# Kernel tuning notes

Hardware: AMD Instinct MI355X
Metric: run time of the kernel (lower is better)

The kernel has to match this reference:

```python
import jax, jax.numpy as jnp
import numpy as np

N = 100000      # nodes
E = 1_600_000   # edges
IN = 128        # in_channels
OUT = 64        # out_channels


def _glorot(k, shape):
    lim = float(np.sqrt(6.0 / (shape[0] + shape[1])))
    return jax.random.uniform(k, shape, jnp.float32, -lim, lim)


def setup_inputs() -> dict:
    key = jax.random.key(0)
    ks = jax.random.split(key, 8)
    x = jax.random.normal(ks[0], (N, IN), jnp.float32)
    edge_index = jax.random.randint(ks[1], (2, E), 0, N, jnp.int32)
    eps = jax.random.normal(ks[2], (N, OUT), jnp.float32)
    return {
        "x": x,
        "edge_index": edge_index,
        "eps": eps,
        "W1": _glorot(ks[3], (IN, OUT)),
        "b1": jnp.zeros((OUT,), jnp.float32),
        "Wmu": _glorot(ks[4], (OUT, OUT)),
        "bmu": jnp.zeros((OUT,), jnp.float32),
        "Wlv": _glorot(ks[5], (OUT, OUT)),
        "blv": jnp.zeros((OUT,), jnp.float32),
        "Wdec": _glorot(ks[6], (OUT, IN)),
        "bdec": jnp.zeros((IN,), jnp.float32),
    }


def gcn_conv(x, W, b, src, dst, n):
    """PyG GCNConv: add self-loops, D^-1/2 (A+I) D^-1/2 X W + b."""
    h = x @ W  # [N, F] transform before aggregation (small F)
    deg = jax.ops.segment_sum(jnp.ones((src.shape[0],), h.dtype), dst,
                              num_segments=n) + 1.0  # +1 for self-loop
    dinv = jax.lax.rsqrt(deg)  # [N]
    norm = dinv[src] * dinv[dst]  # [E]
    msgs = h[src] * norm[:, None]  # [E, F] gather + scale
    agg = jax.ops.segment_sum(msgs, dst, num_segments=n)
    agg = agg + h * (dinv * dinv)[:, None]  # self-loop contribution
    return agg + b


def reference(x, edge_index, eps, W1, b1, Wmu, bmu, Wlv, blv, Wdec, bdec):
    src, dst = edge_index[0], edge_index[1]
    n = x.shape[0]
    h = jax.nn.relu(gcn_conv(x, W1, b1, src, dst, n))
    mu = gcn_conv(h, Wmu, bmu, src, dst, n)
    logvar = gcn_conv(h, Wlv, blv, src, dst, n)
    z = mu + eps * jnp.exp(logvar)  # training-mode reparameterize (std = exp(logvar), per source)
    recon = jax.nn.sigmoid(z @ Wdec + bdec)
    return recon, mu, logvar
```

## Files before the change

### kernel.cpp

```cpp
#include <hip/hip_runtime.h>


static __host__ __device__ inline size_t ws_align(size_t x) { return (x + 255) & ~size_t(255); }

__global__ void k_deg(const int* __restrict__ dst, int E, int* __restrict__ deg) {
    int e = blockIdx.x * blockDim.x + threadIdx.x;
    if (e < E) atomicAdd(&deg[dst[e]], 1);
}

__global__ void k_dinv(const int* __restrict__ deg, int N, float* __restrict__ dinv) {
    int i = blockIdx.x * blockDim.x + threadIdx.x;
    if (i < N) dinv[i] = rsqrtf((float)(deg[i] + 1));
}

__global__ void k_scan_partial(const int* __restrict__ deg, int N, int* __restrict__ part) {
    __shared__ int s[256];
    int t = threadIdx.x;
    int i = blockIdx.x * 256 + t;
    s[t] = (i < N) ? deg[i] : 0;
    __syncthreads();
    for (int off = 128; off > 0; off >>= 1) {
        if (t < off) s[t] += s[t + off];
        __syncthreads();
    }
    if (t == 0) part[blockIdx.x] = s[0];
}

__global__ void k_scan_top(const int* __restrict__ part, int nb, int* __restrict__ scanned) {
    __shared__ int s[512];
    int t = threadIdx.x;
    int v = (t < nb) ? part[t] : 0;
    s[t] = v;
    __syncthreads();
    for (int off = 1; off < 512; off <<= 1) {
        int x = 0;
        if (t >= off) x = s[t - off];
        __syncthreads();
        s[t] += x;
        __syncthreads();
    }
    if (t < nb) scanned[t] = s[t] - v;
}

__global__ void k_scan_down(const int* __restrict__ deg, int N, int E,
                            const int* __restrict__ scanned, int* __restrict__ offsets) {
    __shared__ int s[256];
    int t = threadIdx.x;
    int i = blockIdx.x * 256 + t;
    int v = (i < N) ? deg[i] : 0;
    s[t] = v;
    __syncthreads();
    for (int off = 1; off < 256; off <<= 1) {
        int x = 0;
        if (t >= off) x = s[t - off];
        __syncthreads();
        s[t] += x;
        __syncthreads();
    }
    if (i < N) offsets[i] = scanned[blockIdx.x] + s[t] - v;
    if (blockIdx.x == 0 && t == 0) offsets[N] = E;
}

__global__ void k_scatter(const int* __restrict__ src, const int* __restrict__ dst, int E,
                          int* __restrict__ cursor, int* __restrict__ src_sorted) {
    int e = blockIdx.x * blockDim.x + threadIdx.x;
    if (e < E) {
        int slot = atomicAdd(&cursor[dst[e]], 1);
        src_sorted[slot] = src[e];
    }
}

__global__ __launch_bounds__(256) void k_gemm_in(const float* __restrict__ X,
                                                 const float* __restrict__ W,
                                                 const float* __restrict__ dinv, int N,
                                                 float* __restrict__ C) {
    __shared__ float Ws[128 * 64];
    __shared__ float Xs[16][128];
    int t = threadIdx.x;
    const float4* W4 = (const float4*)W;
    float4* Ws4 = (float4*)Ws;
#pragma unroll
    for (int j = 0; j < 8; j++) Ws4[t + 256 * j] = W4[t + 256 * j];
    int row0 = blockIdx.x * 16;
    const float4* X4 = (const float4*)(X + (size_t)row0 * 128);
    float4* Xs4 = (float4*)&Xs[0][0];
#pragma unroll
    for (int j = 0; j < 2; j++) Xs4[t + 256 * j] = X4[t + 256 * j];
    __syncthreads();
    int r = t >> 4;
    int c0 = (t & 15) * 4;
    float a0 = 0.f, a1 = 0.f, a2 = 0.f, a3 = 0.f;
#pragma unroll 4
    for (int k = 0; k < 128; k++) {
        float xv = Xs[r][k];
        float4 w = *(const float4*)&Ws[k * 64 + c0];
        a0 += xv * w.x; a1 += xv * w.y; a2 += xv * w.z; a3 += xv * w.w;
    }
    float dv = dinv[row0 + r];
    float4 out = {a0 * dv, a1 * dv, a2 * dv, a3 * dv};
    *(float4*)(C + (size_t)(row0 + r) * 64 + c0) = out;
}

template <bool FIRST>
__global__ __launch_bounds__(256) void k_agg(const float* __restrict__ Hs,
                                             const float* __restrict__ dinv,
                                             const int* __restrict__ offsets,
                                             const int* __restrict__ src_sorted,
                                             const float* __restrict__ bias, int N,
                                             float* __restrict__ out) {
    int node = blockIdx.x * 4 + (threadIdx.x >> 6);
    int lane = threadIdx.x & 63;
    if (node >= N) return;
    float dv = dinv[node];
    int beg = offsets[node], end = offsets[node + 1];
    int nu = __builtin_amdgcn_readfirstlane(node);
    float acc = Hs[(size_t)nu * 64 + lane];
    float acc2 = 0.f;
    int j = beg;
    for (; j + 4 <= end; j += 4) {
        int s0 = __builtin_amdgcn_readfirstlane(src_sorted[j + 0]);
        int s1 = __builtin_amdgcn_readfirstlane(src_sorted[j + 1]);
        int s2 = __builtin_amdgcn_readfirstlane(src_sorted[j + 2]);
        int s3 = __builtin_amdgcn_readfirstlane(src_sorted[j + 3]);
        float h0 = Hs[(size_t)s0 * 64 + lane];
        float h1 = Hs[(size_t)s1 * 64 + lane];
        float h2 = Hs[(size_t)s2 * 64 + lane];
        float h3 = Hs[(size_t)s3 * 64 + lane];
        acc += h0 + h1;
        acc2 += h2 + h3;
    }
    for (; j < end; j++) {
        int s = __builtin_amdgcn_readfirstlane(src_sorted[j]);
        acc += Hs[(size_t)s * 64 + lane];
    }
    acc += acc2;
    float v;
    if (FIRST) {
        v = dv * acc + bias[lane];
        v = fmaxf(v, 0.f) * dv;
    } else {
        v = dv * acc;
    }
    out[(size_t)node * 64 + lane] = v;
}

__global__ __launch_bounds__(256) void k_muvz(const float* __restrict__ AGG,
                                              const float* __restrict__ Wmu,
                                              const float* __restrict__ bmu,
                                              const float* __restrict__ Wlv,
                                              const float* __restrict__ blv,
                                              const float* __restrict__ EPS, int N,
                                              float* __restrict__ mu_out,
                                              float* __restrict__ lv_out,
                                              float* __restrict__ z_out) {
    __shared__ float Wm[64 * 64];
    __shared__ float Wl[64 * 64];
    __shared__ float As[16][64];
    int t = threadIdx.x;
#pragma unroll
    for (int j = 0; j < 4; j++) {
        ((float4*)Wm)[t + 256 * j] = ((const float4*)Wmu)[t + 256 * j];
        ((float4*)Wl)[t + 256 * j] = ((const float4*)Wlv)[t + 256 * j];
    }
    int row0 = blockIdx.x * 16;
    ((float4*)&As[0][0])[t] = ((const float4*)(AGG + (size_t)row0 * 64))[t];
    __syncthreads();
    int r = t >> 4;
    int c0 = (t & 15) * 4;
    float m0 = 0.f, m1 = 0.f, m2 = 0.f, m3 = 0.f;
    float l0 = 0.f, l1 = 0.f, l2 = 0.f, l3 = 0.f;
#pragma unroll 4
    for (int k = 0; k < 64; k++) {
        float a = As[r][k];
        float4 wm = *(const float4*)&Wm[k * 64 + c0];
        float4 wl = *(const float4*)&Wl[k * 64 + c0];
        m0 += a * wm.x; m1 += a * wm.y; m2 += a * wm.z; m3 += a * wm.w;
        l0 += a * wl.x; l1 += a * wl.y; l2 += a * wl.z; l3 += a * wl.w;
    }
    size_t base = (size_t)(row0 + r) * 64 + c0;
    float4 bm = *(const float4*)&bmu[c0];
    float4 bl = *(const float4*)&blv[c0];
    float4 ep = *(const float4*)&EPS[base];
    m0 += bm.x; m1 += bm.y; m2 += bm.z; m3 += bm.w;
    l0 += bl.x; l1 += bl.y; l2 += bl.z; l3 += bl.w;
    float z0 = m0 + ep.x * expf(l0);
    float z1 = m1 + ep.y * expf(l1);
    float z2 = m2 + ep.z * expf(l2);
    float z3 = m3 + ep.w * expf(l3);
    *(float4*)&mu_out[base] = {m0, m1, m2, m3};
    *(float4*)&lv_out[base] = {l0, l1, l2, l3};
    *(float4*)&z_out[base] = {z0, z1, z2, z3};
}

__global__ __launch_bounds__(256) void k_dec(const float* __restrict__ Z,
                                             const float* __restrict__ Wdec,
                                             const float* __restrict__ bdec, int N,
                                             float* __restrict__ recon) {
    __shared__ float Ws[64 * 128];
    __shared__ float Zs[16][64];
    int t = threadIdx.x;
#pragma unroll
    for (int j = 0; j < 8; j++)
        ((float4*)Ws)[t + 256 * j] = ((const float4*)Wdec)[t + 256 * j];
    int row0 = blockIdx.x * 16;
    ((float4*)&Zs[0][0])[t] = ((const float4*)(Z + (size_t)row0 * 64))[t];
    __syncthreads();
    int r = t >> 4;
    int c0 = (t & 15) * 8;
    float a[8] = {0.f, 0.f, 0.f, 0.f, 0.f, 0.f, 0.f, 0.f};
#pragma unroll 4
    for (int k = 0; k < 64; k++) {
        float zv = Zs[r][k];
        float4 w0 = *(const float4*)&Ws[k * 128 + c0];
        float4 w1 = *(const float4*)&Ws[k * 128 + c0 + 4];
        a[0] += zv * w0.x; a[1] += zv * w0.y; a[2] += zv * w0.z; a[3] += zv * w0.w;
        a[4] += zv * w1.x; a[5] += zv * w1.y; a[6] += zv * w1.z; a[7] += zv * w1.w;
    }
    size_t base = (size_t)(row0 + r) * 128 + c0;
    float4 b0 = *(const float4*)&bdec[c0];
    float4 b1 = *(const float4*)&bdec[c0 + 4];
    float v0 = a[0] + b0.x, v1 = a[1] + b0.y, v2 = a[2] + b0.z, v3 = a[3] + b0.w;
    float v4 = a[4] + b1.x, v5 = a[5] + b1.y, v6 = a[6] + b1.z, v7 = a[7] + b1.w;
    float4 o0 = {1.f / (1.f + expf(-v0)), 1.f / (1.f + expf(-v1)),
                 1.f / (1.f + expf(-v2)), 1.f / (1.f + expf(-v3))};
    float4 o1 = {1.f / (1.f + expf(-v4)), 1.f / (1.f + expf(-v5)),
                 1.f / (1.f + expf(-v6)), 1.f / (1.f + expf(-v7))};
    *(float4*)&recon[base] = o0;
    *(float4*)&recon[base + 4] = o1;
}

extern "C" void kernel_launch(void* const* d_in, const int* in_sizes, int n_in,
                              void* d_out, int out_size, void* d_ws, size_t ws_size,
                              hipStream_t stream) {
    const float* x = (const float*)d_in[0];
    const int* edge_index = (const int*)d_in[1];
    const float* eps = (const float*)d_in[2];
    const float* W1 = (const float*)d_in[3];
    const float* b1 = (const float*)d_in[4];
    const float* Wmu = (const float*)d_in[5];
    const float* bmu = (const float*)d_in[6];
    const float* Wlv = (const float*)d_in[7];
    const float* blv = (const float*)d_in[8];
    const float* Wdec = (const float*)d_in[9];
    const float* bdec = (const float*)d_in[10];

    int N = in_sizes[0] / 128;
    int E = in_sizes[1] / 2;
    const int* src = edge_index;
    const int* dst = edge_index + E;

    float* recon = (float*)d_out;
    float* mu_out = (float*)d_out + (size_t)N * 128;
    float* lv_out = mu_out + (size_t)N * 64;

    char* p = (char*)d_ws;
    auto alloc = [&](size_t bytes) { char* r = p; p += ws_align(bytes); return r; };
    int nb = (N + 255) / 256;
    int* deg = (int*)alloc((size_t)N * 4);
    float* dinv = (float*)alloc((size_t)N * 4);
    int* offsets = (int*)alloc((size_t)(N + 1) * 4);
    int* cursor = (int*)alloc((size_t)N * 4);
    int* part = (int*)alloc((size_t)nb * 4);
    int* scanned = (int*)alloc((size_t)nb * 4);
    int* src_sorted = (int*)alloc((size_t)E * 4);
    float* bufA = (float*)alloc((size_t)N * 64 * 4);
    float* bufB = (float*)alloc((size_t)N * 64 * 4);

    hipMemsetAsync(deg, 0, (size_t)N * 4, stream);

    const int tpb = 256;
    k_deg<<<(E + tpb - 1) / tpb, tpb, 0, stream>>>(dst, E, deg);
    k_dinv<<<(N + tpb - 1) / tpb, tpb, 0, stream>>>(deg, N, dinv);
    k_scan_partial<<<nb, 256, 0, stream>>>(deg, N, part);
    k_scan_top<<<1, 512, 0, stream>>>(part, nb, scanned);
    k_scan_down<<<nb, 256, 0, stream>>>(deg, N, E, scanned, offsets);
    hipMemcpyAsync(cursor, offsets, (size_t)N * 4, hipMemcpyDeviceToDevice, stream);
    k_scatter<<<(E + tpb - 1) / tpb, tpb, 0, stream>>>(src, dst, E, cursor, src_sorted);

    k_gemm_in<<<N / 16, 256, 0, stream>>>(x, W1, dinv, N, bufA);
    k_agg<true><<<(N + 3) / 4, 256, 0, stream>>>(bufA, dinv, offsets, src_sorted, b1, N, bufB);
    k_agg<false><<<(N + 3) / 4, 256, 0, stream>>>(bufB, dinv, offsets, src_sorted, nullptr, N, bufA);
    k_muvz<<<N / 16, 256, 0, stream>>>(bufA, Wmu, bmu, Wlv, blv, eps, N, mu_out, lv_out, bufB);
    k_dec<<<N / 16, 256, 0, stream>>>(bufB, Wdec, bdec, N, recon);
}
```

Measured before the change: 619.6 us.

## Replace per-node CSR sort with bucketed edge sort and LDS-atomic aggregation

Swaps the per-destination CSR build for a coarse counting sort into 256-node buckets. That build was a global-atomic degree pass, a three-kernel scan, a device copy and a scatter using global atomics. The new sort uses per-block shared-memory histograms, a single-block scan and a scatter with shared-memory cursors. Each edge is packed into one int (local destination in the high bits, source in the low 17 bits). Aggregation now runs one 512-thread block per bucket that accumulates into a 64 KB LDS tile with float atomics, instead of a wave per node summing in registers. The trade-off is far fewer, larger blocks, which means lower occupancy for the latency-bound gather, plus LDS atomic contention. The constants are also tied to the problem size: 98 blocks of 16384 edges, 391 buckets, and node ids below 2^17.

```diff
diff --git a/kernel.cpp b/kernel.cpp
--- a/kernel.cpp
+++ b/kernel.cpp
@@ -1,11 +1,30 @@
 #include <hip/hip_runtime.h>
 
 
+#define NBNODES 256
+#define NBUCKETS 391
+#define EPB 16384
+#define NBLK 98
+
 static __host__ __device__ inline size_t ws_align(size_t x) { return (x + 255) & ~size_t(255); }
 
-__global__ void k_deg(const int* __restrict__ dst, int E, int* __restrict__ deg) {
-    int e = blockIdx.x * blockDim.x + threadIdx.x;
-    if (e < E) atomicAdd(&deg[dst[e]], 1);
+__global__ __launch_bounds__(512) void k_hist(const int* __restrict__ dst, int E,
+                                              int* __restrict__ hist_g, int* __restrict__ deg) {
+    __shared__ int hist[NBUCKETS];
+    int t = threadIdx.x;
+    if (t < NBUCKETS) hist[t] = 0;
+    __syncthreads();
+    int base = blockIdx.x * EPB;
+    for (int i = t; i < EPB; i += 512) {
+        int e = base + i;
+        if (e < E) {
+            int d = dst[e];
+            atomicAdd(&hist[d >> 8], 1);
+            atomicAdd(&deg[d], 1);
+        }
+    }
+    __syncthreads();
+    if (t < NBUCKETS) hist_g[t * NBLK + blockIdx.x] = hist[t];
 }
 
 __global__ void k_dinv(const int* __restrict__ deg, int N, float* __restrict__ dinv) {
@@ -13,24 +32,20 @@
     if (i < N) dinv[i] = rsqrtf((float)(deg[i] + 1));
 }
 
-__global__ void k_scan_partial(const int* __restrict__ deg, int N, int* __restrict__ part) {
-    __shared__ int s[256];
-    int t = threadIdx.x;
-    int i = blockIdx.x * 256 + t;
-    s[t] = (i < N) ? deg[i] : 0;
-    __syncthreads();
-    for (int off = 128; off > 0; off >>= 1) {
-        if (t < off) s[t] += s[t + off];
-        __syncthreads();
-    }
-    if (t == 0) part[blockIdx.x] = s[0];
-}
-
-__global__ void k_scan_top(const int* __restrict__ part, int nb, int* __restrict__ scanned) {
+__global__ __launch_bounds__(512) void k_scan(int* __restrict__ hist_g, int E,
+                                              int* __restrict__ bstart) {
     __shared__ int s[512];
     int t = threadIdx.x;
-    int v = (t < nb) ? part[t] : 0;
-    s[t] = v;
+    int total = 0;
+    if (t < NBUCKETS) {
+        int* row = hist_g + t * NBLK;
+        for (int k = 0; k < NBLK; k++) {
+            int c = row[k];
+            row[k] = total;
+            total += c;
+        }
+    }
+    s[t] = total;
     __syncthreads();
     for (int off = 1; off < 512; off <<= 1) {
         int x = 0;
@@ -39,34 +54,32 @@
         s[t] += x;
         __syncthreads();
     }
-    if (t < nb) scanned[t] = s[t] - v;
-}
-
-__global__ void k_scan_down(const int* __restrict__ deg, int N, int E,
-                            const int* __restrict__ scanned, int* __restrict__ offsets) {
-    __shared__ int s[256];
-    int t = threadIdx.x;
-    int i = blockIdx.x * 256 + t;
-    int v = (i < N) ? deg[i] : 0;
-    s[t] = v;
-    __syncthreads();
-    for (int off = 1; off < 256; off <<= 1) {
-        int x = 0;
-        if (t >= off) x = s[t - off];
-        __syncthreads();
-        s[t] += x;
-        __syncthreads();
-    }
-    if (i < N) offsets[i] = scanned[blockIdx.x] + s[t] - v;
-    if (blockIdx.x == 0 && t == 0) offsets[N] = E;
-}
-
-__global__ void k_scatter(const int* __restrict__ src, const int* __restrict__ dst, int E,
-                          int* __restrict__ cursor, int* __restrict__ src_sorted) {
-    int e = blockIdx.x * blockDim.x + threadIdx.x;
-    if (e < E) {
-        int slot = atomicAdd(&cursor[dst[e]], 1);
-        src_sorted[slot] = src[e];
+    int start = s[t] - total;
+    if (t < NBUCKETS) {
+        bstart[t] = start;
+        int* row = hist_g + t * NBLK;
+        for (int k = 0; k < NBLK; k++) row[k] += start;
+    }
+    if (t == 0) bstart[NBUCKETS] = E;
+}
+
+__global__ __launch_bounds__(512) void k_scatter(const int* __restrict__ src,
+                                                 const int* __restrict__ dst, int E,
+                                                 const int* __restrict__ hist_g,
+                                                 int* __restrict__ ebuf) {
+    __shared__ int cur[NBUCKETS];
+    int t = threadIdx.x;
+    if (t < NBUCKETS) cur[t] = hist_g[t * NBLK + blockIdx.x];
+    __syncthreads();
+    int base = blockIdx.x * EPB;
+    for (int i = t; i < EPB; i += 512) {
+        int e = base + i;
+        if (e < E) {
+            int d = dst[e];
+            int sv = src[e];
+            int slot = atomicAdd(&cur[d >> 8], 1);
+            ebuf[slot] = ((d & 255) << 17) | sv;
+        }
     }
 }
 
@@ -102,46 +115,77 @@
 }
 
 template <bool FIRST>
-__global__ __launch_bounds__(256) void k_agg(const float* __restrict__ Hs,
-                                             const float* __restrict__ dinv,
-                                             const int* __restrict__ offsets,
-                                             const int* __restrict__ src_sorted,
-                                             const float* __restrict__ bias, int N,
-                                             float* __restrict__ out) {
-    int node = blockIdx.x * 4 + (threadIdx.x >> 6);
-    int lane = threadIdx.x & 63;
-    if (node >= N) return;
-    float dv = dinv[node];
-    int beg = offsets[node], end = offsets[node + 1];
-    int nu = __builtin_amdgcn_readfirstlane(node);
-    float acc = Hs[(size_t)nu * 64 + lane];
-    float acc2 = 0.f;
-    int j = beg;
-    for (; j + 4 <= end; j += 4) {
-        int s0 = __builtin_amdgcn_readfirstlane(src_sorted[j + 0]);
-        int s1 = __builtin_amdgcn_readfirstlane(src_sorted[j + 1]);
-        int s2 = __builtin_amdgcn_readfirstlane(src_sorted[j + 2]);
-        int s3 = __builtin_amdgcn_readfirstlane(src_sorted[j + 3]);
-        float h0 = Hs[(size_t)s0 * 64 + lane];
-        float h1 = Hs[(size_t)s1 * 64 + lane];
-        float h2 = Hs[(size_t)s2 * 64 + lane];
-        float h3 = Hs[(size_t)s3 * 64 + lane];
-        acc += h0 + h1;
-        acc2 += h2 + h3;
-    }
-    for (; j < end; j++) {
-        int s = __builtin_amdgcn_readfirstlane(src_sorted[j]);
-        acc += Hs[(size_t)s * 64 + lane];
-    }
-    acc += acc2;
-    float v;
-    if (FIRST) {
-        v = dv * acc + bias[lane];
-        v = fmaxf(v, 0.f) * dv;
-    } else {
-        v = dv * acc;
-    }
-    out[(size_t)node * 64 + lane] = v;
+__global__ __launch_bounds__(512) void k_aggb(const float* __restrict__ Hs,
+                                              const float* __restrict__ dinv,
+                                              const int* __restrict__ bstart,
+                                              const int* __restrict__ ebuf,
+                                              const float* __restrict__ bias, int N,
+                                              float* __restrict__ out) {
+    __shared__ float acc[NBNODES * 64];
+    int b = blockIdx.x;
+    int nb0 = b << 8;
+    int nn = min(NBNODES, N - nb0);
+    int t = threadIdx.x;
+    float4* a4 = (float4*)acc;
+    const float4* H4 = (const float4*)(Hs + (size_t)nb0 * 64);
+    for (int i = t; i < nn * 16; i += 512) a4[i] = H4[i];
+    __syncthreads();
+    int beg = bstart[b], end = bstart[b + 1];
+    int cnt = end - beg;
+    int wave = t >> 6, lane = t & 63;
+    int chunk = (cnt + 7) >> 3;
+    int j0 = beg + wave * chunk;
+    int j1 = min(j0 + chunk, end);
+    int j = j0;
+    for (; j + 8 <= j1; j += 8) {
+        int e0 = __builtin_amdgcn_readfirstlane(ebuf[j + 0]);
+        int e1 = __builtin_amdgcn_readfirstlane(ebuf[j + 1]);
+        int e2 = __builtin_amdgcn_readfirstlane(ebuf[j + 2]);
+        int e3 = __builtin_amdgcn_readfirstlane(ebuf[j + 3]);
+        int e4 = __builtin_amdgcn_readfirstlane(ebuf[j + 4]);
+        int e5 = __builtin_amdgcn_readfirstlane(ebuf[j + 5]);
+        int e6 = __builtin_amdgcn_readfirstlane(ebuf[j + 6]);
+        int e7 = __builtin_amdgcn_readfirstlane(ebuf[j + 7]);
+        float v0 = Hs[(size_t)(e0 & 0x1FFFF) * 64 + lane];
+        float v1 = Hs[(size_t)(e1 & 0x1FFFF) * 64 + lane];
+        float v2 = Hs[(size_t)(e2 & 0x1FFFF) * 64 + lane];
+        float v3 = Hs[(size_t)(e3 & 0x1FFFF) * 64 + lane];
+        float v4 = Hs[(size_t)(e4 & 0x1FFFF) * 64 + lane];
+        float v5 = Hs[(size_t)(e5 & 0x1FFFF) * 64 + lane];
+        float v6 = Hs[(size_t)(e6 & 0x1FFFF) * 64 + lane];
+        float v7 = Hs[(size_t)(e7 & 0x1FFFF) * 64 + lane];
+        atomicAdd(&acc[((unsigned)e0 >> 17) * 64 + lane], v0);
+        atomicAdd(&acc[((unsigned)e1 >> 17) * 64 + lane], v1);
+        atomicAdd(&acc[((unsigned)e2 >> 17) * 64 + lane], v2);
+        atomicAdd(&acc[((unsigned)e3 >> 17) * 64 + lane], v3);
+        atomicAdd(&acc[((unsigned)e4 >> 17) * 64 + lane], v4);
+        atomicAdd(&acc[((unsigned)e5 >> 17) * 64 + lane], v5);
+        atomicAdd(&acc[((unsigned)e6 >> 17) * 64 + lane], v6);
+        atomicAdd(&acc[((unsigned)e7 >> 17) * 64 + lane], v7);
+    }
+    for (; j < j1; j++) {
+        int e0 = __builtin_amdgcn_readfirstlane(ebuf[j]);
+        float v0 = Hs[(size_t)(e0 & 0x1FFFF) * 64 + lane];
+        atomicAdd(&acc[((unsigned)e0 >> 17) * 64 + lane], v0);
+    }
+    __syncthreads();
+    float4* o4 = (float4*)(out + (size_t)nb0 * 64);
+    for (int i = t; i < nn * 16; i += 512) {
+        int row = i >> 4;
+        float dv = dinv[nb0 + row];
+        float4 v = a4[i];
+        if (FIRST) {
+            int q = i & 15;
+            float4 bb = ((const float4*)bias)[q];
+            v.x = fmaxf(dv * v.x + bb.x, 0.f) * dv;
+            v.y = fmaxf(dv * v.y + bb.y, 0.f) * dv;
+            v.z = fmaxf(dv * v.z + bb.z, 0.f) * dv;
+            v.w = fmaxf(dv * v.w + bb.w, 0.f) * dv;
+        } else {
+            v.x *= dv; v.y *= dv; v.z *= dv; v.w *= dv;
+        }
+        o4[i] = v;
+    }
 }
 
 __global__ __launch_bounds__(256) void k_muvz(const float* __restrict__ AGG,
@@ -255,31 +299,24 @@
 
     char* p = (char*)d_ws;
     auto alloc = [&](size_t bytes) { char* r = p; p += ws_align(bytes); return r; };
-    int nb = (N + 255) / 256;
     int* deg = (int*)alloc((size_t)N * 4);
     float* dinv = (float*)alloc((size_t)N * 4);
-    int* offsets = (int*)alloc((size_t)(N + 1) * 4);
-    int* cursor = (int*)alloc((size_t)N * 4);
-    int* part = (int*)alloc((size_t)nb * 4);
-    int* scanned = (int*)alloc((size_t)nb * 4);
-    int* src_sorted = (int*)alloc((size_t)E * 4);
+    int* hist_g = (int*)alloc((size_t)NBUCKETS * NBLK * 4);
+    int* bstart = (int*)alloc((size_t)(NBUCKETS + 1) * 4);
+    int* ebuf = (int*)alloc((size_t)E * 4);
     float* bufA = (float*)alloc((size_t)N * 64 * 4);
     float* bufB = (float*)alloc((size_t)N * 64 * 4);
 
     hipMemsetAsync(deg, 0, (size_t)N * 4, stream);
 
-    const int tpb = 256;
-    k_deg<<<(E + tpb - 1) / tpb, tpb, 0, stream>>>(dst, E, deg);
-    k_dinv<<<(N + tpb - 1) / tpb, tpb, 0, stream>>>(deg, N, dinv);
-    k_scan_partial<<<nb, 256, 0, stream>>>(deg, N, part);
-    k_scan_top<<<1, 512, 0, stream>>>(part, nb, scanned);
-    k_scan_down<<<nb, 256, 0, stream>>>(deg, N, E, scanned, offsets);
-    hipMemcpyAsync(cursor, offsets, (size_t)N * 4, hipMemcpyDeviceToDevice, stream);
-    k_scatter<<<(E + tpb - 1) / tpb, tpb, 0, stream>>>(src, dst, E, cursor, src_sorted);
+    k_hist<<<NBLK, 512, 0, stream>>>(dst, E, hist_g, deg);
+    k_dinv<<<(N + 255) / 256, 256, 0, stream>>>(deg, N, dinv);
+    k_scan<<<1, 512, 0, stream>>>(hist_g, E, bstart);
+    k_scatter<<<NBLK, 512, 0, stream>>>(src, dst, E, hist_g, ebuf);
 
     k_gemm_in<<<N / 16, 256, 0, stream>>>(x, W1, dinv, N, bufA);
-    k_agg<true><<<(N + 3) / 4, 256, 0, stream>>>(bufA, dinv, offsets, src_sorted, b1, N, bufB);
-    k_agg<false><<<(N + 3) / 4, 256, 0, stream>>>(bufB, dinv, offsets, src_sorted, nullptr, N, bufA);
+    k_aggb<true><<<NBUCKETS, 512, 0, stream>>>(bufA, dinv, bstart, ebuf, b1, N, bufB);
+    k_aggb<false><<<NBUCKETS, 512, 0, stream>>>(bufB, dinv, bstart, ebuf, nullptr, N, bufA);
     k_muvz<<<N / 16, 256, 0, stream>>>(bufA, Wmu, bmu, Wlv, blv, eps, N, mu_out, lv_out, bufB);
     k_dec<<<N / 16, 256, 0, stream>>>(bufB, Wdec, bdec, N, recon);
 }
```

Result: slower. 1.788 ms (+188.6%).
